# Kernel tuning notes

Measured on AMD Instinct MI355X. Metric: run time of the kernel, lower is better.

## Reference

```python
import jax, jax.numpy as jnp
from jax import lax
import numpy as np

B, A, D = 4, 512, 729   # batch, num_angles, detector pixels
H, W = 512, 512         # reconstruction volume


def setup_inputs() -> dict:
    key = jax.random.key(0)
    sino = jax.random.normal(key, (B, A, D), dtype=jnp.float32)
    vol_spacing = np.array([1.0, 1.0], dtype=np.float32)          # (sy, sx)
    det_spacing = np.array([1.0], dtype=np.float32)
    vol_origin = np.array([-(H - 1) / 2.0, -(W - 1) / 2.0], dtype=np.float32)
    det_origin = np.array([-(D - 1) / 2.0], dtype=np.float32)
    angles = jnp.linspace(0.0, jnp.pi, A, endpoint=False, dtype=jnp.float32)
    return {
        "input": sino,
        "volume_shape": np.array([H, W], dtype=np.int64),
        "volume_origin": jnp.asarray(vol_origin),
        "detector_origin": jnp.asarray(det_origin),
        "volume_spacing": jnpp if False else jnp.asarray(vol_spacing),
        "detector_spacing": jnp.asarray(det_spacing),
        "trajectory": angles,
    }


def _backproject(sino, vol_shape, vol_origin, det_origin, vol_spacing, det_spacing, angles):
    h, w = int(vol_shape[0]), int(vol_shape[1])
    d = sino.shape[-1]
    ys = vol_origin[0] + jnp.arange(h, dtype=sino.dtype) * vol_spacing[0]  # [H]
    xs = vol_origin[1] + jnp.arange(w, dtype=sino.dtype) * vol_spacing[1]  # [W]

    def step(acc, per_angle):
        theta, sino_a = per_angle                      # scalar, [B, D]
        # ray coordinate s = x*cos(theta) + y*sin(theta) for every voxel
        s = xs[None, :] * jnp.cos(theta) + ys[:, None] * jnp.sin(theta)  # [H, W]
        u = (s - det_origin[0]) / det_spacing[0]       # continuous detector index
        u0 = jnp.floor(u)
        frac = u - u0
        i0 = u0.astype(jnp.int32)
        i1 = i0 + 1
        valid0 = (i0 >= 0) & (i0 < d)
        valid1 = (i1 >= 0) & (i1 < d)
        i0c = jnp.clip(i0, 0, d - 1)
        i1c = jnp.clip(i1, 0, d - 1)
        v0 = sino_a[:, i0c]                            # [B, H, W] gather
        v1 = sino_a[:, i1c]                            # [B, H, W] gather
        contrib = (jnp.where(valid0, (1.0 - frac) * v0, 0.0)
                   + jnp.where(valid1, frac * v1, 0.0))
        return acc + contrib, None

    acc0 = jnp.zeros((sino.shape[0], h, w), dtype=sino.dtype)
    out, _ = lax.scan(step, acc0, (angles, jnp.swapaxes(sino, 0, 1)))
    return out


def reference(input, volume_shape, volume_origin, detector_origin,
              volume_spacing, detector_spacing, trajectory):
    return _backproject(input, volume_shape, volume_origin, detector_origin,
                        volume_spacing, detector_spacing, trajectory)
```

## Files before the change

kernel.cpp:

```cpp
#include <hip/hip_runtime.h>
#include <hip/hip_fp16.h>

#define BB 4
#define AA 512
#define ZS 8
#define AH (AA / ZS)
#define DD 729
#define HH 512
#define WW 512
#define CH 4
#define NC (AH / CH)
#define WIN 32
#define GX (WW / 64)
#define GY (HH / 16)

typedef float        f4v  __attribute__((ext_vector_type(4)));
typedef unsigned int u4v8 __attribute__((ext_vector_type(4), aligned(8)));

__device__ inline float buf_load1(__amdgpu_buffer_rsrc_t r, int elem) {
    union { unsigned int u; float f; } c;
    c.u = __builtin_amdgcn_raw_buffer_load_b32(r, elem * 4, 0, 0);
    return c.f;
}
__device__ inline __half2 h2bc(unsigned int x) {
    return __builtin_bit_cast(__half2, x);
}
__device__ inline unsigned int pk2u(float a, float b) {
    return __builtin_bit_cast(unsigned int, __builtin_amdgcn_cvt_pkrtz(a, b));
}

__global__ __launch_bounds__(256, 8) void bp_kernel(
    const float* __restrict__ sino,
    const float* __restrict__ vol_origin,
    const float* __restrict__ det_origin,
    const float* __restrict__ vol_spacing,
    const float* __restrict__ det_spacing,
    const float* __restrict__ angles,
    float* __restrict__ out)
{
    __shared__ f4v          s_csk[4][AH];
    __shared__ int          s_s0[4][AH];
    __shared__ unsigned int s_win[4][CH * WIN * 2];

    const int tid  = threadIdx.y * 16 + threadIdx.x;
    const int lane = tid & 63;
    const int wv   = tid >> 6;

    const int nlin = (int)blockIdx.x + GX * ((int)blockIdx.y + GY * (int)blockIdx.z);
    const int zsl  = nlin & (ZS - 1);
    const int mm   = nlin >> 3;
    const int bxx  = mm & (GX - 1);
    const int byy  = mm >> 3;

    const float inv_ds = 1.0f / det_spacing[0];
    const int abase = zsl * AH;

    const int x0 = bxx * 64 + wv * 16;
    const int y0 = byy * 16;
    const float vsx = vol_spacing[1], vsy = vol_spacing[0];
    const float off = -det_origin[0] * inv_ds;
    const float xc = vol_origin[1] + ((float)x0 + 7.5f) * vsx;
    const float yc = vol_origin[0] + ((float)y0 + 7.5f) * vsy;

    {
        const int a = lane;
        float th = angles[abase + a];
        float c = cosf(th) * inv_ds;
        float s = sinf(th) * inv_ds;
        float uc = fmaf(xc, c, fmaf(yc, s, off));
        int s0 = min(max((int)uc - (WIN / 2), 0), DD - WIN);
        f4v k;
        k.x = c; k.y = s; k.z = off - (float)s0; k.w = 4.0f * vsy * s;
        s_csk[wv][a] = k;
        s_s0[wv][a]  = s0;
    }
    __threadfence_block();

    const int ix  = x0 + threadIdx.x;
    const int iy0 = y0 + (threadIdx.y & 3);
    const float xw = vol_origin[1] + (float)ix * vsx;
    const float yw = vol_origin[0] + (float)iy0 * vsy;

    const int hh = lane & 1;
    const int ee = lane >> 1;
    const int gA = (2 * hh) * (AA * DD) + ee;

    const __amdgpu_buffer_rsrc_t rsrc = __builtin_amdgcn_make_buffer_rsrc(
        (void*)sino, (short)0, BB * AA * DD * 4, 0x00020000);

    f4v acc0 = {0.f, 0.f, 0.f, 0.f};
    f4v acc1 = {0.f, 0.f, 0.f, 0.f};
    f4v acc2 = {0.f, 0.f, 0.f, 0.f};
    f4v acc3 = {0.f, 0.f, 0.f, 0.f};

    const __half2 hz   = h2bc(0u);
    const __half2 one2 = h2bc(0x3C003C00u);
    __half2 h01_0 = hz, h23_0 = hz, h01_1 = hz, h23_1 = hz;
    __half2 h01_2 = hz, h23_2 = hz, h01_3 = hz, h23_3 = hz;

    float vA0, vB0, vA1, vB1, vA2, vB2, vA3, vB3;

    #define STAGE_LOAD(C)                                                  \
        do {                                                               \
            const int aa = (C) * CH;                                       \
            const int r0 = (abase + aa + 0) * DD + s_s0[wv][aa + 0] + gA;  \
            const int r1 = (abase + aa + 1) * DD + s_s0[wv][aa + 1] + gA;  \
            const int r2 = (abase + aa + 2) * DD + s_s0[wv][aa + 2] + gA;  \
            const int r3 = (abase + aa + 3) * DD + s_s0[wv][aa + 3] + gA;  \
            vA0 = buf_load1(rsrc, r0); vB0 = buf_load1(rsrc, r0 + AA * DD);\
            vA1 = buf_load1(rsrc, r1); vB1 = buf_load1(rsrc, r1 + AA * DD);\
            vA2 = buf_load1(rsrc, r2); vB2 = buf_load1(rsrc, r2 + AA * DD);\
            vA3 = buf_load1(rsrc, r3); vB3 = buf_load1(rsrc, r3 + AA * DD);\
        } while (0)

    #define CONVERT_WRITE()                                                \
        do {                                                               \
            s_win[wv][0 * 64 + lane] = pk2u(vA0, vB0);                     \
            s_win[wv][1 * 64 + lane] = pk2u(vA1, vB1);                     \
            s_win[wv][2 * 64 + lane] = pk2u(vA2, vB2);                     \
            s_win[wv][3 * 64 + lane] = pk2u(vA3, vB3);                     \
        } while (0)

    #define LERP(U, H01, H23)                                              \
        do {                                                               \
            const int   li = (int)(U);                                     \
            const float fr = __builtin_amdgcn_fractf(U);                   \
            const __half2 fr2 = h2bc(pk2u(fr, fr));                        \
            const __half2 om2 = __hsub2(one2, fr2);                        \
            const u4v8 t = *(const u4v8*)&s_win[wv][(j * WIN + li) * 2];   \
            H01 = __hfma2(h2bc(t.x), om2, __hfma2(h2bc(t.z), fr2, H01));   \
            H23 = __hfma2(h2bc(t.y), om2, __hfma2(h2bc(t.w), fr2, H23));   \
        } while (0)

    #define WIDEN(H01, H23, ACC)                                           \
        do {                                                               \
            (ACC).x += __low2float(H01);  (ACC).y += __high2float(H01);    \
            (ACC).z += __low2float(H23);  (ACC).w += __high2float(H23);    \
            H01 = hz; H23 = hz;                                            \
        } while (0)

    STAGE_LOAD(0);
    for (int c = 0; c < NC; ++c) {
        __threadfence_block();
        CONVERT_WRITE();
        __threadfence_block();
        if (c + 1 < NC) STAGE_LOAD(c + 1);
        #pragma unroll
        for (int j = 0; j < CH; ++j) {
            const f4v  k  = s_csk[wv][c * CH + j];
            const float u0 = fmaf(xw, k.x, fmaf(yw, k.y, k.z));
            const float u1 = u0 + k.w;
            const float u2 = u1 + k.w;
            const float u3 = u2 + k.w;
            LERP(u0, h01_0, h23_0);
            LERP(u1, h01_1, h23_1);
            LERP(u2, h01_2, h23_2);
            LERP(u3, h01_3, h23_3);
        }
        WIDEN(h01_0, h23_0, acc0);
        WIDEN(h01_1, h23_1, acc1);
        WIDEN(h01_2, h23_2, acc2);
        WIDEN(h01_3, h23_3, acc3);
    }
    #undef STAGE_LOAD
    #undef CONVERT_WRITE
    #undef LERP
    #undef WIDEN

    const size_t HW = (size_t)HH * WW;
    #define OUT4(ACC, ROWOFF)                                              \
        do {                                                               \
            const size_t o = (size_t)(iy0 + (ROWOFF)) * WW + ix;           \
            unsafeAtomicAdd(&out[o],          (ACC).x);                    \
            unsafeAtomicAdd(&out[o + HW],     (ACC).y);                    \
            unsafeAtomicAdd(&out[o + 2 * HW], (ACC).z);                    \
            unsafeAtomicAdd(&out[o + 3 * HW], (ACC).w);                    \
        } while (0)
    OUT4(acc0, 0);
    OUT4(acc1, 4);
    OUT4(acc2, 8);
    OUT4(acc3, 12);
    #undef OUT4
}

extern "C" void kernel_launch(void* const* d_in, const int* in_sizes, int n_in,
                              void* d_out, int out_size, void* d_ws, size_t ws_size,
                              hipStream_t stream) {
    const float* sino        = (const float*)d_in[0];
    const float* vol_origin  = (const float*)d_in[2];
    const float* det_origin  = (const float*)d_in[3];
    const float* vol_spacing = (const float*)d_in[4];
    const float* det_spacing = (const float*)d_in[5];
    const float* angles      = (const float*)d_in[6];
    float* out = (float*)d_out;

    hipMemsetAsync(d_out, 0, (size_t)out_size * sizeof(float), stream);

    dim3 block(16, 16, 1);
    dim3 grid(GX, GY, ZS);
    bp_kernel<<<grid, block, 0, stream>>>(sino, vol_origin, det_origin,
                                          vol_spacing, det_spacing, angles, out);
}
```

Before: 121.1 us.

## Double rows per wave with wider 64-pixel detector window per angle

Result: slower. 127.4 us (+5.2%).

```diff
diff --git a/kernel.cpp b/kernel.cpp
--- a/kernel.cpp
+++ b/kernel.cpp
@@ -10,12 +10,14 @@
 #define WW 512
 #define CH 4
 #define NC (AH / CH)
-#define WIN 32
+#define WIN 64
+#define AD (AA * DD)
 #define GX (WW / 64)
-#define GY (HH / 16)
+#define GY (HH / 32)
 
 typedef float        f4v  __attribute__((ext_vector_type(4)));
 typedef unsigned int u4v8 __attribute__((ext_vector_type(4), aligned(8)));
+typedef unsigned int u2v8 __attribute__((ext_vector_type(2), aligned(8)));
 
 __device__ inline float buf_load1(__amdgpu_buffer_rsrc_t r, int elem) {
     union { unsigned int u; float f; } c;
@@ -29,7 +31,7 @@
     return __builtin_bit_cast(unsigned int, __builtin_amdgcn_cvt_pkrtz(a, b));
 }
 
-__global__ __launch_bounds__(256, 8) void bp_kernel(
+__global__ __launch_bounds__(256, 4) void bp_kernel(
     const float* __restrict__ sino,
     const float* __restrict__ vol_origin,
     const float* __restrict__ det_origin,
@@ -40,7 +42,7 @@
 {
     __shared__ f4v          s_csk[4][AH];
     __shared__ int          s_s0[4][AH];
-    __shared__ unsigned int s_win[4][CH * WIN * 2];
+    __shared__ __align__(16) unsigned int s_win[4][CH * WIN * 2];
 
     const int tid  = threadIdx.y * 16 + threadIdx.x;
     const int lane = tid & 63;
@@ -56,11 +58,11 @@
     const int abase = zsl * AH;
 
     const int x0 = bxx * 64 + wv * 16;
-    const int y0 = byy * 16;
+    const int y0 = byy * 32;
     const float vsx = vol_spacing[1], vsy = vol_spacing[0];
     const float off = -det_origin[0] * inv_ds;
     const float xc = vol_origin[1] + ((float)x0 + 7.5f) * vsx;
-    const float yc = vol_origin[0] + ((float)y0 + 7.5f) * vsy;
+    const float yc = vol_origin[0] + ((float)y0 + 15.5f) * vsy;
 
     {
         const int a = lane;
@@ -81,44 +83,52 @@
     const float xw = vol_origin[1] + (float)ix * vsx;
     const float yw = vol_origin[0] + (float)iy0 * vsy;
 
-    const int hh = lane & 1;
-    const int ee = lane >> 1;
-    const int gA = (2 * hh) * (AA * DD) + ee;
-
     const __amdgpu_buffer_rsrc_t rsrc = __builtin_amdgcn_make_buffer_rsrc(
         (void*)sino, (short)0, BB * AA * DD * 4, 0x00020000);
 
-    f4v acc0 = {0.f, 0.f, 0.f, 0.f};
-    f4v acc1 = {0.f, 0.f, 0.f, 0.f};
-    f4v acc2 = {0.f, 0.f, 0.f, 0.f};
-    f4v acc3 = {0.f, 0.f, 0.f, 0.f};
+    f4v acc0 = {0.f,0.f,0.f,0.f}, acc1 = {0.f,0.f,0.f,0.f};
+    f4v acc2 = {0.f,0.f,0.f,0.f}, acc3 = {0.f,0.f,0.f,0.f};
+    f4v acc4 = {0.f,0.f,0.f,0.f}, acc5 = {0.f,0.f,0.f,0.f};
+    f4v acc6 = {0.f,0.f,0.f,0.f}, acc7 = {0.f,0.f,0.f,0.f};
 
     const __half2 hz   = h2bc(0u);
     const __half2 one2 = h2bc(0x3C003C00u);
     __half2 h01_0 = hz, h23_0 = hz, h01_1 = hz, h23_1 = hz;
     __half2 h01_2 = hz, h23_2 = hz, h01_3 = hz, h23_3 = hz;
-
-    float vA0, vB0, vA1, vB1, vA2, vB2, vA3, vB3;
+    __half2 h01_4 = hz, h23_4 = hz, h01_5 = hz, h23_5 = hz;
+    __half2 h01_6 = hz, h23_6 = hz, h01_7 = hz, h23_7 = hz;
+
+    float vA0, vA1, vA2, vA3, vB0, vB1, vB2, vB3;
+    float vC0, vC1, vC2, vC3, vD0, vD1, vD2, vD3;
 
     #define STAGE_LOAD(C)                                                  \
         do {                                                               \
             const int aa = (C) * CH;                                       \
-            const int r0 = (abase + aa + 0) * DD + s_s0[wv][aa + 0] + gA;  \
-            const int r1 = (abase + aa + 1) * DD + s_s0[wv][aa + 1] + gA;  \
-            const int r2 = (abase + aa + 2) * DD + s_s0[wv][aa + 2] + gA;  \
-            const int r3 = (abase + aa + 3) * DD + s_s0[wv][aa + 3] + gA;  \
-            vA0 = buf_load1(rsrc, r0); vB0 = buf_load1(rsrc, r0 + AA * DD);\
-            vA1 = buf_load1(rsrc, r1); vB1 = buf_load1(rsrc, r1 + AA * DD);\
-            vA2 = buf_load1(rsrc, r2); vB2 = buf_load1(rsrc, r2 + AA * DD);\
-            vA3 = buf_load1(rsrc, r3); vB3 = buf_load1(rsrc, r3 + AA * DD);\
+            const int r0 = (abase + aa + 0) * DD + s_s0[wv][aa + 0] + lane;\
+            const int r1 = (abase + aa + 1) * DD + s_s0[wv][aa + 1] + lane;\
+            const int r2 = (abase + aa + 2) * DD + s_s0[wv][aa + 2] + lane;\
+            const int r3 = (abase + aa + 3) * DD + s_s0[wv][aa + 3] + lane;\
+            vA0 = buf_load1(rsrc, r0);          vA1 = buf_load1(rsrc, r0 + AD);     \
+            vA2 = buf_load1(rsrc, r0 + 2 * AD); vA3 = buf_load1(rsrc, r0 + 3 * AD); \
+            vB0 = buf_load1(rsrc, r1);          vB1 = buf_load1(rsrc, r1 + AD);     \
+            vB2 = buf_load1(rsrc, r1 + 2 * AD); vB3 = buf_load1(rsrc, r1 + 3 * AD); \
+            vC0 = buf_load1(rsrc, r2);          vC1 = buf_load1(rsrc, r2 + AD);     \
+            vC2 = buf_load1(rsrc, r2 + 2 * AD); vC3 = buf_load1(rsrc, r2 + 3 * AD); \
+            vD0 = buf_load1(rsrc, r3);          vD1 = buf_load1(rsrc, r3 + AD);     \
+            vD2 = buf_load1(rsrc, r3 + 2 * AD); vD3 = buf_load1(rsrc, r3 + 3 * AD); \
         } while (0)
 
     #define CONVERT_WRITE()                                                \
         do {                                                               \
-            s_win[wv][0 * 64 + lane] = pk2u(vA0, vB0);                     \
-            s_win[wv][1 * 64 + lane] = pk2u(vA1, vB1);                     \
-            s_win[wv][2 * 64 + lane] = pk2u(vA2, vB2);                     \
-            s_win[wv][3 * 64 + lane] = pk2u(vA3, vB3);                     \
+            u2v8 q;                                                        \
+            q.x = pk2u(vA0, vA1); q.y = pk2u(vA2, vA3);                    \
+            *(u2v8*)&s_win[wv][0 * 128 + 2 * lane] = q;                    \
+            q.x = pk2u(vB0, vB1); q.y = pk2u(vB2, vB3);                    \
+            *(u2v8*)&s_win[wv][1 * 128 + 2 * lane] = q;                    \
+            q.x = pk2u(vC0, vC1); q.y = pk2u(vC2, vC3);                    \
+            *(u2v8*)&s_win[wv][2 * 128 + 2 * lane] = q;                    \
+            q.x = pk2u(vD0, vD1); q.y = pk2u(vD2, vD3);                    \
+            *(u2v8*)&s_win[wv][3 * 128 + 2 * lane] = q;                    \
         } while (0)
 
     #define LERP(U, H01, H23)                                              \
@@ -147,20 +157,25 @@
         if (c + 1 < NC) STAGE_LOAD(c + 1);
         #pragma unroll
         for (int j = 0; j < CH; ++j) {
-            const f4v  k  = s_csk[wv][c * CH + j];
-            const float u0 = fmaf(xw, k.x, fmaf(yw, k.y, k.z));
-            const float u1 = u0 + k.w;
-            const float u2 = u1 + k.w;
-            const float u3 = u2 + k.w;
-            LERP(u0, h01_0, h23_0);
-            LERP(u1, h01_1, h23_1);
-            LERP(u2, h01_2, h23_2);
-            LERP(u3, h01_3, h23_3);
+            const f4v k = s_csk[wv][c * CH + j];
+            float u = fmaf(xw, k.x, fmaf(yw, k.y, k.z));
+            LERP(u, h01_0, h23_0); u += k.w;
+            LERP(u, h01_1, h23_1); u += k.w;
+            LERP(u, h01_2, h23_2); u += k.w;
+            LERP(u, h01_3, h23_3); u += k.w;
+            LERP(u, h01_4, h23_4); u += k.w;
+            LERP(u, h01_5, h23_5); u += k.w;
+            LERP(u, h01_6, h23_6); u += k.w;
+            LERP(u, h01_7, h23_7);
         }
         WIDEN(h01_0, h23_0, acc0);
         WIDEN(h01_1, h23_1, acc1);
         WIDEN(h01_2, h23_2, acc2);
         WIDEN(h01_3, h23_3, acc3);
+        WIDEN(h01_4, h23_4, acc4);
+        WIDEN(h01_5, h23_5, acc5);
+        WIDEN(h01_6, h23_6, acc6);
+        WIDEN(h01_7, h23_7, acc7);
     }
     #undef STAGE_LOAD
     #undef CONVERT_WRITE
@@ -180,6 +195,10 @@
     OUT4(acc1, 4);
     OUT4(acc2, 8);
     OUT4(acc3, 12);
+    OUT4(acc4, 16);
+    OUT4(acc5, 20);
+    OUT4(acc6, 24);
+    OUT4(acc7, 28);
     #undef OUT4
 }
 
```
